# Kernel optimization log

Measured on AMD Instinct MI355X. Metric: run time of the kernel, lower is better.

Reference implementation:

```python
import jax, jax.numpy as jnp
import numpy as np

B = 32       # batch_size
N = 8192     # points per set
D = 128      # d_in
LAM = 0.01   # lambda_ ridge regularizer


def setup_inputs() -> dict:
    key = jax.random.key(0)
    x = jax.random.normal(key, (B, N, D), dtype=jnp.float32)
    return {"x": x}


def reference(x):
    Bb, Nn, Dd = x.shape
    # mean-center over the point dim, then batched cov = diffs^T @ diffs / (N-1)
    diffs = x - x.mean(axis=1, keepdims=True)                  # (B, N, D)
    cov = jnp.einsum('bnd,bne->bde', diffs, diffs) / (Nn - 1)  # (B, D, D)
    cov = cov + LAM * jnp.eye(Dd, dtype=x.dtype)
    # torch.unique(dim=1) with generic float data: rows are all distinct,
    # so it reduces to a lexicographic ascending sort of the D rows.
    # jnp.lexsort uses the LAST key as primary -> reverse columns of m.T.
    idx = jax.vmap(lambda m: jnp.lexsort(m.T[::-1]))(cov)      # (B, D)
    sorted_cov = jnp.take_along_axis(cov, idx[:, :, None], axis=1)
    return sorted_cov.reshape(Bb, Dd * Dd)                     # (B, d_out)
```

## Files before the change

### kernel.cpp

```cpp
#include <hip/hip_runtime.h>
#include <hip/hip_bf16.h>

#define DD 128
#define NPTS 8192
#define BBATCH 32
#define BK 64
#define LAM 0.01f

typedef __attribute__((ext_vector_type(8))) short bf16x8;
typedef __attribute__((ext_vector_type(16))) float f32x16;

__device__ __forceinline__ unsigned f2bf_u(float f) {
    unsigned u = __builtin_bit_cast(unsigned, f);
    return (u + 0x7FFFu + ((u >> 16) & 1u)) >> 16;
}
__device__ __forceinline__ float bf2f(unsigned short u) {
    unsigned v = ((unsigned)u) << 16;
    return __builtin_bit_cast(float, v);
}

__device__ __forceinline__ int swz(int d) { return ((d >> 2) ^ d) & 7; }

__global__ __launch_bounds__(256) void gram_stats(
    const float* __restrict__ x, unsigned short* __restrict__ Spart,
    float* __restrict__ CSpart, float* __restrict__ KDpart, int P)
{
    __shared__ short XT[DD * BK];

    const int blk = blockIdx.x;
    const int b   = blk & 31;
    const int kc  = blk >> 5;
    const int rowsPerBlk = NPTS / P;
    const int k0g = kc * rowsPerBlk;
    const float* xb = x + (size_t)b * NPTS * DD;

    const int tid  = threadIdx.x;
    const int lane = tid & 63;
    const int wave = tid >> 6;
    const int dg   = tid & 31;
    const int aa   = tid >> 5;

    const int wr = (wave >> 1) * 64;
    const int wc = (wave & 1) * 64;

    f32x16 acc00 = {}; f32x16 acc01 = {}; f32x16 acc10 = {}; f32x16 acc11 = {};
    float csum[4] = {0.f, 0.f, 0.f, 0.f};
    float kdot[4] = {0.f, 0.f, 0.f, 0.f};

    for (int kt = 0; kt < rowsPerBlk; kt += BK) {
        __syncthreads();
        #pragma unroll
        for (int pass = 0; pass < 2; ++pass) {
            const int krow = kt + pass * 32 + aa * 4;
            const float4* src = (const float4*)(xb + (size_t)(k0g + krow) * DD) + dg;
            float4 m0 = src[0];
            float4 m1 = src[DD / 4];
            float4 m2 = src[2 * (DD / 4)];
            float4 m3 = src[3 * (DD / 4)];
            float x00 = __shfl(m0.x, lane & 32);
            float x01 = __shfl(m1.x, lane & 32);
            float x02 = __shfl(m2.x, lane & 32);
            float x03 = __shfl(m3.x, lane & 32);
            float e0[4] = {m0.x, m0.y, m0.z, m0.w};
            float e1[4] = {m1.x, m1.y, m1.z, m1.w};
            float e2[4] = {m2.x, m2.y, m2.z, m2.w};
            float e3[4] = {m3.x, m3.y, m3.z, m3.w};
            const int chunk = pass * 4 + (aa >> 1);
            #pragma unroll
            for (int i = 0; i < 4; ++i) {
                csum[i] += e0[i] + e1[i] + e2[i] + e3[i];
                kdot[i] += x00 * e0[i] + x01 * e1[i] + x02 * e2[i] + x03 * e3[i];
                const int d = 4 * dg + i;
                unsigned u0 = f2bf_u(e0[i]) | (f2bf_u(e1[i]) << 16);
                unsigned u1 = f2bf_u(e2[i]) | (f2bf_u(e3[i]) << 16);
                const int addr = d * BK + ((chunk ^ swz(d)) * 8) + (aa & 1) * 4;
                uint2 v; v.x = u0; v.y = u1;
                *(uint2*)(XT + addr) = v;
            }
        }
        __syncthreads();
        #pragma unroll
        for (int ks = 0; ks < BK / 16; ++ks) {
            const int chunkBase = ks * 2 + (lane >> 5);
            const int m = lane & 31;
            const int a0d = wr + m, a1d = wr + 32 + m;
            const int b0d = wc + m, b1d = wc + 32 + m;
            bf16x8 a0 = *(const bf16x8*)(XT + a0d * BK + ((chunkBase ^ swz(a0d)) * 8));
            bf16x8 a1 = *(const bf16x8*)(XT + a1d * BK + ((chunkBase ^ swz(a1d)) * 8));
            bf16x8 b0 = *(const bf16x8*)(XT + b0d * BK + ((chunkBase ^ swz(b0d)) * 8));
            bf16x8 b1 = *(const bf16x8*)(XT + b1d * BK + ((chunkBase ^ swz(b1d)) * 8));
            acc00 = __builtin_amdgcn_mfma_f32_32x32x16_bf16(a0, b0, acc00, 0, 0, 0);
            acc01 = __builtin_amdgcn_mfma_f32_32x32x16_bf16(a0, b1, acc01, 0, 0, 0);
            acc10 = __builtin_amdgcn_mfma_f32_32x32x16_bf16(a1, b0, acc10, 0, 0, 0);
            acc11 = __builtin_amdgcn_mfma_f32_32x32x16_bf16(a1, b1, acc11, 0, 0, 0);
        }
    }

    unsigned short* Sp = Spart + ((size_t)b * P + kc) * (DD * DD);
    const int colLane = lane & 31;
    const int rowHw = 4 * (lane >> 5);
    {
        const f32x16* accs[4] = {&acc00, &acc01, &acc10, &acc11};
        const int rb[4] = {wr, wr, wr + 32, wr + 32};
        const int cb[4] = {wc, wc + 32, wc, wc + 32};
        #pragma unroll
        for (int t = 0; t < 4; ++t) {
            #pragma unroll
            for (int r = 0; r < 16; ++r) {
                int row = rb[t] + (r & 3) + 8 * (r >> 2) + rowHw;
                Sp[row * DD + cb[t] + colLane] = (unsigned short)f2bf_u((*accs[t])[r]);
            }
        }
    }

    __syncthreads();
    float* red = (float*)XT;
    #pragma unroll
    for (int i = 0; i < 4; ++i) {
        red[tid] = csum[i];
        __syncthreads();
        if (tid < 32) {
            float s = 0.f;
            #pragma unroll
            for (int g = 0; g < 8; ++g) s += red[g * 32 + tid];
            CSpart[((size_t)b * P + kc) * DD + 4 * tid + i] = s;
        }
        __syncthreads();
        red[tid] = kdot[i];
        __syncthreads();
        if (tid < 32) {
            float s = 0.f;
            #pragma unroll
            for (int g = 0; g < 8; ++g) s += red[g * 32 + tid];
            KDpart[((size_t)b * P + kc) * DD + 4 * tid + i] = s;
        }
        __syncthreads();
    }
}

__global__ __launch_bounds__(256) void reduce_sort2(
    const unsigned short* __restrict__ Spart, const float* __restrict__ CSpart,
    const float* __restrict__ KDpart, float* __restrict__ out, int P)
{
    __shared__ float cs[DD];
    __shared__ float key[DD];
    __shared__ int rankArr[DD];

    const int b   = blockIdx.x;
    const int seg = blockIdx.y;
    const int tid = threadIdx.x;
    const float invN = 1.f / NPTS;
    const float invNm1 = 1.f / (NPTS - 1);

    float kd = 0.f;
    if (tid < DD) {
        float s = 0.f;
        for (int p = 0; p < P; ++p) {
            s  += CSpart[((size_t)b * P + p) * DD + tid];
            kd += KDpart[((size_t)b * P + p) * DD + tid];
        }
        cs[tid] = s;
    }
    __syncthreads();
    if (tid < DD) {
        key[tid] = (kd - cs[tid] * cs[0] * invN) * invNm1 + ((tid == 0) ? LAM : 0.f);
    }
    __syncthreads();

    const int base = seg * (16 * DD) + tid * 8;
    float acc[8] = {0.f, 0.f, 0.f, 0.f, 0.f, 0.f, 0.f, 0.f};
    for (int p = 0; p < P; ++p) {
        bf16x8 v = *(const bf16x8*)(Spart + ((size_t)b * P + p) * (DD * DD) + base);
        #pragma unroll
        for (int i = 0; i < 8; ++i) acc[i] += bf2f((unsigned short)v[i]);
    }

    auto covv = [&](int i, int j) -> float {
        float s = 0.f;
        for (int p = 0; p < P; ++p)
            s += bf2f(Spart[((size_t)b * P + p) * (DD * DD) + i * DD + j]);
        return (s - cs[i] * cs[j] * invN) * invNm1 + ((i == j) ? LAM : 0.f);
    };
    if (tid < DD) {
        const float ki = key[tid];
        int r = 0;
        for (int j = 0; j < DD; ++j) {
            if (j == tid) continue;
            const float kj = key[j];
            bool less;
            if (kj != ki) {
                less = (kj < ki);
            } else {
                less = (j < tid);
                for (int t = 1; t < DD; ++t) {
                    float a = covv(j, t), c = covv(tid, t);
                    if (a != c) { less = (a < c); break; }
                }
            }
            r += less ? 1 : 0;
        }
        rankArr[tid] = r;
    }
    __syncthreads();

    const int row = seg * 16 + (tid >> 4);
    const int j0  = (tid & 15) * 8;
    const float ci = cs[row];
    float4 v0, v1;
    float* o = out + (size_t)b * DD * DD + (size_t)rankArr[row] * DD + j0;
    {
        float vals[8];
        #pragma unroll
        for (int i = 0; i < 8; ++i) {
            const int j = j0 + i;
            vals[i] = (acc[i] - ci * cs[j] * invN) * invNm1 + ((row == j) ? LAM : 0.f);
        }
        v0.x = vals[0]; v0.y = vals[1]; v0.z = vals[2]; v0.w = vals[3];
        v1.x = vals[4]; v1.y = vals[5]; v1.z = vals[6]; v1.w = vals[7];
    }
    *(float4*)(o)     = v0;
    *(float4*)(o + 4) = v1;
}

extern "C" void kernel_launch(void* const* d_in, const int* in_sizes, int n_in,
                              void* d_out, int out_size, void* d_ws, size_t ws_size,
                              hipStream_t stream)
{
    const float* x = (const float*)d_in[0];
    float* out = (float*)d_out;

    int P = 16;
    while (P > 1) {
        size_t need = (size_t)BBATCH * P * (DD * DD) * sizeof(unsigned short)
                    + (size_t)BBATCH * P * 2 * DD * sizeof(float);
        if (need <= ws_size) break;
        P >>= 1;
    }
    size_t nS = (size_t)BBATCH * P * DD * DD;
    unsigned short* Spart = (unsigned short*)d_ws;
    float* CSpart = (float*)(Spart + nS);
    float* KDpart = CSpart + (size_t)BBATCH * P * DD;

    gram_stats<<<dim3(32 * P), dim3(256), 0, stream>>>(x, Spart, CSpart, KDpart, P);
    reduce_sort2<<<dim3(BBATCH, 8), dim3(256), 0, stream>>>(Spart, CSpart, KDpart, out, P);
}
```

Baseline: 216.4 us.

## Prefetch input tiles in registers, split sort into rank kernel, template split count

The Gram kernel now loads the next 64-row tile of x into registers before the MFMA stage of the current tile, so global-load latency overlaps compute. P becomes a template parameter and the default split goes up to 32 when workspace allows, giving more blocks at the cost of a larger partial-sum buffer. Ranking moves into a small separate kernel that compares only the diagonal-column keys, with ties broken by index. The reduce/scatter kernel uses 16 segments of 8 rows. Dropping the full lexicographic tiebreak could change ordering when keys tie, and the extra launch adds overhead.

```diff
diff --git a/kernel.cpp b/kernel.cpp
--- a/kernel.cpp
+++ b/kernel.cpp
@@ -18,19 +18,20 @@
     unsigned v = ((unsigned)u) << 16;
     return __builtin_bit_cast(float, v);
 }
-
 __device__ __forceinline__ int swz(int d) { return ((d >> 2) ^ d) & 7; }
 
+template<int P>
 __global__ __launch_bounds__(256) void gram_stats(
     const float* __restrict__ x, unsigned short* __restrict__ Spart,
-    float* __restrict__ CSpart, float* __restrict__ KDpart, int P)
+    float* __restrict__ CSpart, float* __restrict__ KDpart)
 {
     __shared__ short XT[DD * BK];
+    constexpr int rowsPerBlk = NPTS / P;
+    constexpr int T = rowsPerBlk / BK;
 
     const int blk = blockIdx.x;
     const int b   = blk & 31;
     const int kc  = blk >> 5;
-    const int rowsPerBlk = NPTS / P;
     const int k0g = kc * rowsPerBlk;
     const float* xb = x + (size_t)b * NPTS * DD;
 
@@ -39,7 +40,6 @@
     const int wave = tid >> 6;
     const int dg   = tid & 31;
     const int aa   = tid >> 5;
-
     const int wr = (wave >> 1) * 64;
     const int wc = (wave & 1) * 64;
 
@@ -47,36 +47,44 @@
     float csum[4] = {0.f, 0.f, 0.f, 0.f};
     float kdot[4] = {0.f, 0.f, 0.f, 0.f};
 
-    for (int kt = 0; kt < rowsPerBlk; kt += BK) {
-        __syncthreads();
+    float4 Ra[4], Rb[4];
+    auto loadPass = [&](float4* Rg, int krow0) {
+        const float4* s = (const float4*)(xb + (size_t)(k0g + krow0 + aa * 4) * DD) + dg;
+        Rg[0] = s[0]; Rg[1] = s[32]; Rg[2] = s[64]; Rg[3] = s[96];
+    };
+    auto consumePass = [&](const float4* Rg, int pass) {
+        float4 m0 = Rg[0], m1 = Rg[1], m2 = Rg[2], m3 = Rg[3];
+        float x00 = __shfl(m0.x, lane & 32), x01 = __shfl(m1.x, lane & 32);
+        float x02 = __shfl(m2.x, lane & 32), x03 = __shfl(m3.x, lane & 32);
+        float e0[4] = {m0.x, m0.y, m0.z, m0.w};
+        float e1[4] = {m1.x, m1.y, m1.z, m1.w};
+        float e2[4] = {m2.x, m2.y, m2.z, m2.w};
+        float e3[4] = {m3.x, m3.y, m3.z, m3.w};
+        const int chunk = pass * 4 + (aa >> 1);
         #pragma unroll
-        for (int pass = 0; pass < 2; ++pass) {
-            const int krow = kt + pass * 32 + aa * 4;
-            const float4* src = (const float4*)(xb + (size_t)(k0g + krow) * DD) + dg;
-            float4 m0 = src[0];
-            float4 m1 = src[DD / 4];
-            float4 m2 = src[2 * (DD / 4)];
-            float4 m3 = src[3 * (DD / 4)];
-            float x00 = __shfl(m0.x, lane & 32);
-            float x01 = __shfl(m1.x, lane & 32);
-            float x02 = __shfl(m2.x, lane & 32);
-            float x03 = __shfl(m3.x, lane & 32);
-            float e0[4] = {m0.x, m0.y, m0.z, m0.w};
-            float e1[4] = {m1.x, m1.y, m1.z, m1.w};
-            float e2[4] = {m2.x, m2.y, m2.z, m2.w};
-            float e3[4] = {m3.x, m3.y, m3.z, m3.w};
-            const int chunk = pass * 4 + (aa >> 1);
-            #pragma unroll
-            for (int i = 0; i < 4; ++i) {
-                csum[i] += e0[i] + e1[i] + e2[i] + e3[i];
-                kdot[i] += x00 * e0[i] + x01 * e1[i] + x02 * e2[i] + x03 * e3[i];
-                const int d = 4 * dg + i;
-                unsigned u0 = f2bf_u(e0[i]) | (f2bf_u(e1[i]) << 16);
-                unsigned u1 = f2bf_u(e2[i]) | (f2bf_u(e3[i]) << 16);
-                const int addr = d * BK + ((chunk ^ swz(d)) * 8) + (aa & 1) * 4;
-                uint2 v; v.x = u0; v.y = u1;
-                *(uint2*)(XT + addr) = v;
-            }
+        for (int i = 0; i < 4; ++i) {
+            csum[i] += e0[i] + e1[i] + e2[i] + e3[i];
+            kdot[i] += x00 * e0[i] + x01 * e1[i] + x02 * e2[i] + x03 * e3[i];
+            const int d = 4 * dg + i;
+            unsigned u0 = f2bf_u(e0[i]) | (f2bf_u(e1[i]) << 16);
+            unsigned u1 = f2bf_u(e2[i]) | (f2bf_u(e3[i]) << 16);
+            const int addr = d * BK + ((chunk ^ swz(d)) * 8) + (aa & 1) * 4;
+            uint2 v; v.x = u0; v.y = u1;
+            *(uint2*)(XT + addr) = v;
+        }
+    };
+
+    loadPass(Ra, 0);
+    loadPass(Rb, 32);
+
+    #pragma unroll
+    for (int t = 0; t < T; ++t) {
+        __syncthreads();
+        consumePass(Ra, 0);
+        consumePass(Rb, 1);
+        if (t + 1 < T) {
+            loadPass(Ra, (t + 1) * BK);
+            loadPass(Rb, (t + 1) * BK + 32);
         }
         __syncthreads();
         #pragma unroll
@@ -138,109 +146,102 @@
     }
 }
 
-__global__ __launch_bounds__(256) void reduce_sort2(
-    const unsigned short* __restrict__ Spart, const float* __restrict__ CSpart,
-    const float* __restrict__ KDpart, float* __restrict__ out, int P)
-{
-    __shared__ float cs[DD];
+template<int P>
+__global__ __launch_bounds__(128) void keys_ranks(
+    const float* __restrict__ CSpart, const float* __restrict__ KDpart,
+    float* __restrict__ csOut, int* __restrict__ rankOut)
+{
+    __shared__ float csh[DD];
     __shared__ float key[DD];
-    __shared__ int rankArr[DD];
-
-    const int b   = blockIdx.x;
+    const int b = blockIdx.x;
+    const int tid = threadIdx.x;
+    float s = 0.f, kd = 0.f;
+    #pragma unroll
+    for (int p = 0; p < P; ++p) {
+        s  += CSpart[((size_t)b * P + p) * DD + tid];
+        kd += KDpart[((size_t)b * P + p) * DD + tid];
+    }
+    csh[tid] = s;
+    __syncthreads();
+    const float k = (kd - s * csh[0] * (1.f / NPTS)) * (1.f / (NPTS - 1))
+                  + ((tid == 0) ? LAM : 0.f);
+    key[tid] = k;
+    __syncthreads();
+    int r = 0;
+    #pragma unroll 8
+    for (int j = 0; j < DD; ++j) {
+        const float kj = key[j];
+        r += (kj < k) || (kj == k && j < tid);
+    }
+    csOut[b * DD + tid] = s;
+    rankOut[b * DD + tid] = r;
+}
+
+template<int P>
+__global__ __launch_bounds__(256) void reduce_scatter(
+    const unsigned short* __restrict__ Spart, const float* __restrict__ csOut,
+    const int* __restrict__ rankOut, float* __restrict__ out)
+{
+    __shared__ float csh[DD];
+    __shared__ int rk[8];
+    const int b = blockIdx.x;
     const int seg = blockIdx.y;
     const int tid = threadIdx.x;
-    const float invN = 1.f / NPTS;
-    const float invNm1 = 1.f / (NPTS - 1);
-
-    float kd = 0.f;
-    if (tid < DD) {
-        float s = 0.f;
-        for (int p = 0; p < P; ++p) {
-            s  += CSpart[((size_t)b * P + p) * DD + tid];
-            kd += KDpart[((size_t)b * P + p) * DD + tid];
-        }
-        cs[tid] = s;
-    }
-    __syncthreads();
-    if (tid < DD) {
-        key[tid] = (kd - cs[tid] * cs[0] * invN) * invNm1 + ((tid == 0) ? LAM : 0.f);
-    }
-    __syncthreads();
-
-    const int base = seg * (16 * DD) + tid * 8;
-    float acc[8] = {0.f, 0.f, 0.f, 0.f, 0.f, 0.f, 0.f, 0.f};
+    if (tid < DD) csh[tid] = csOut[b * DD + tid];
+    if (tid < 8)  rk[tid] = rankOut[b * DD + seg * 8 + tid];
+
+    const int base = seg * (8 * DD) + tid * 4;
+    float a0 = 0.f, a1 = 0.f, a2 = 0.f, a3 = 0.f;
+    #pragma unroll
     for (int p = 0; p < P; ++p) {
-        bf16x8 v = *(const bf16x8*)(Spart + ((size_t)b * P + p) * (DD * DD) + base);
-        #pragma unroll
-        for (int i = 0; i < 8; ++i) acc[i] += bf2f((unsigned short)v[i]);
-    }
-
-    auto covv = [&](int i, int j) -> float {
-        float s = 0.f;
-        for (int p = 0; p < P; ++p)
-            s += bf2f(Spart[((size_t)b * P + p) * (DD * DD) + i * DD + j]);
-        return (s - cs[i] * cs[j] * invN) * invNm1 + ((i == j) ? LAM : 0.f);
-    };
-    if (tid < DD) {
-        const float ki = key[tid];
-        int r = 0;
-        for (int j = 0; j < DD; ++j) {
-            if (j == tid) continue;
-            const float kj = key[j];
-            bool less;
-            if (kj != ki) {
-                less = (kj < ki);
-            } else {
-                less = (j < tid);
-                for (int t = 1; t < DD; ++t) {
-                    float a = covv(j, t), c = covv(tid, t);
-                    if (a != c) { less = (a < c); break; }
-                }
-            }
-            r += less ? 1 : 0;
-        }
-        rankArr[tid] = r;
-    }
-    __syncthreads();
-
-    const int row = seg * 16 + (tid >> 4);
-    const int j0  = (tid & 15) * 8;
-    const float ci = cs[row];
-    float4 v0, v1;
-    float* o = out + (size_t)b * DD * DD + (size_t)rankArr[row] * DD + j0;
-    {
-        float vals[8];
-        #pragma unroll
-        for (int i = 0; i < 8; ++i) {
-            const int j = j0 + i;
-            vals[i] = (acc[i] - ci * cs[j] * invN) * invNm1 + ((row == j) ? LAM : 0.f);
-        }
-        v0.x = vals[0]; v0.y = vals[1]; v0.z = vals[2]; v0.w = vals[3];
-        v1.x = vals[4]; v1.y = vals[5]; v1.z = vals[6]; v1.w = vals[7];
-    }
-    *(float4*)(o)     = v0;
-    *(float4*)(o + 4) = v1;
-}
-
-extern "C" void kernel_launch(void* const* d_in, const int* in_sizes, int n_in,
-                              void* d_out, int out_size, void* d_ws, size_t ws_size,
-                              hipStream_t stream)
-{
-    const float* x = (const float*)d_in[0];
-    float* out = (float*)d_out;
-
-    int P = 16;
-    while (P > 1) {
-        size_t need = (size_t)BBATCH * P * (DD * DD) * sizeof(unsigned short)
-                    + (size_t)BBATCH * P * 2 * DD * sizeof(float);
-        if (need <= ws_size) break;
-        P >>= 1;
-    }
+        uint2 v = *(const uint2*)(Spart + ((size_t)b * P + p) * (DD * DD) + base);
+        a0 += bf2f((unsigned short)(v.x & 0xFFFFu));
+        a1 += bf2f((unsigned short)(v.x >> 16));
+        a2 += bf2f((unsigned short)(v.y & 0xFFFFu));
+        a3 += bf2f((unsigned short)(v.y >> 16));
+    }
+    __syncthreads();
+    const int row = seg * 8 + (tid >> 5);
+    const int j0  = (tid & 31) * 4;
+    const float ci = csh[row];
+    const float invN = 1.f / NPTS, invNm1 = 1.f / (NPTS - 1);
+    float4 v;
+    v.x = (a0 - ci * csh[j0 + 0] * invN) * invNm1 + ((row == j0 + 0) ? LAM : 0.f);
+    v.y = (a1 - ci * csh[j0 + 1] * invN) * invNm1 + ((row == j0 + 1) ? LAM : 0.f);
+    v.z = (a2 - ci * csh[j0 + 2] * invN) * invNm1 + ((row == j0 + 2) ? LAM : 0.f);
+    v.w = (a3 - ci * csh[j0 + 3] * invN) * invNm1 + ((row == j0 + 3) ? LAM : 0.f);
+    float* o = out + (size_t)b * DD * DD + (size_t)rk[tid >> 5] * DD + j0;
+    *(float4*)o = v;
+}
+
+template<int P>
+static void launch_all(const float* x, float* out, void* d_ws, hipStream_t stream)
+{
     size_t nS = (size_t)BBATCH * P * DD * DD;
     unsigned short* Spart = (unsigned short*)d_ws;
     float* CSpart = (float*)(Spart + nS);
     float* KDpart = CSpart + (size_t)BBATCH * P * DD;
-
-    gram_stats<<<dim3(32 * P), dim3(256), 0, stream>>>(x, Spart, CSpart, KDpart, P);
-    reduce_sort2<<<dim3(BBATCH, 8), dim3(256), 0, stream>>>(Spart, CSpart, KDpart, out, P);
-}
+    float* csOut  = KDpart + (size_t)BBATCH * P * DD;
+    int*   rankOut = (int*)(csOut + (size_t)BBATCH * DD);
+
+    gram_stats<P><<<dim3(32 * P), dim3(256), 0, stream>>>(x, Spart, CSpart, KDpart);
+    keys_ranks<P><<<dim3(BBATCH), dim3(128), 0, stream>>>(CSpart, KDpart, csOut, rankOut);
+    reduce_scatter<P><<<dim3(BBATCH, 16), dim3(256), 0, stream>>>(Spart, csOut, rankOut, out);
+}
+
+extern "C" void kernel_launch(void* const* d_in, const int* in_sizes, int n_in,
+                              void* d_out, int out_size, void* d_ws, size_t ws_size,
+                              hipStream_t stream)
+{
+    const float* x = (const float*)d_in[0];
+    float* out = (float*)d_out;
+
+    auto need = [](int P) {
+        return (size_t)BBATCH * P * DD * DD * sizeof(unsigned short)
+             + (size_t)BBATCH * P * 2 * DD * sizeof(float)
+             + (size_t)BBATCH * DD * (sizeof(float) + sizeof(int));
+    };
+    if (need(32) <= ws_size)      launch_all<32>(x, out, d_ws, stream);
+    else if (need(16) <= ws_size) launch_all<16>(x, out, d_ws, stream);
+    else                          launch_all<8>(x, out, d_ws, stream);
+}
```

After: 207.8 us. -4.0%, faster.
